# Kernel optimization log

Hardware: AMD Instinct MI355X
Metric: run time of the kernel (lower is better)

The kernel has to match this reference:

```python
import jax, jax.numpy as jnp
import numpy as np

B, D, NB, E, DT, K, TS = 16384, 512, 8, 4, 256, 8, 16
GH = max(D // 2, 16)            # gate hidden = 256
SH = max(int(DT * 0.5), 16)     # safe head hidden = 128
SPD = DT + TS                   # spec head input = 272
SPH = max(int(SPD * 0.25), 16)  # spec hidden = 68
CFD = DT + 1 + 3 + TS + 1 + 1   # conf input = 278
CFH = max(int(CFD * 0.25), 16)  # conf hidden = 69


def _ln(x, g, b):
    m = x.mean(-1, keepdims=True)
    v = ((x - m) ** 2).mean(-1, keepdims=True)
    return (x - m) / jnp.sqrt(v + 1e-5) * g + b


def _resmlp(x, lg, lb, W1, b1, W2, b2):
    h = jax.nn.relu(_ln(x, lg, lb) @ W1 + b1)
    return h @ W2 + b2


def setup_inputs() -> dict:
    key = jax.random.key(0)
    ks = iter(jax.random.split(key, 48))

    def n(shape, s=0.02):
        return (jax.random.normal(next(ks), shape, jnp.float32) * s).astype(jnp.float32)

    inp = {
        'x_num': jax.random.normal(next(ks), (B, D), jnp.float32),
        # GGPLNumericEmbedding
        'basis_weight': n((D, NB + 1, E), 0.001),
        'basis_bias': jnp.zeros((D, E), jnp.float32),
        'bp_min': jnp.zeros((D, 1), jnp.float32),
        'bp_delta_raw': n((D, NB), 0.1),
        'proj_W': n((D * E, D)), 'proj_b': jnp.zeros((D,), jnp.float32),
        # input gate MLP
        'gate_W1': n((D, GH)), 'gate_b1': jnp.zeros((GH,), jnp.float32),
        'gate_W2': n((GH, D)), 'gate_b2': jnp.zeros((D,), jnp.float32),
        # backbone stand-in (TMLPBackbone.encode_hidden): 2-layer MLP -> d_token
        'bb_W1': n((D, DT)), 'bb_b1': jnp.zeros((DT,), jnp.float32),
        'bb_W2': n((DT, DT)), 'bb_b2': jnp.zeros((DT,), jnp.float32),
        # base head
        'base_W': n((DT, 1)), 'base_b': jnp.zeros((1,), jnp.float32),
        # safe residual head (zero_last=True -> zero last weight)
        'safe_ln_g': jnp.ones((DT,), jnp.float32), 'safe_ln_b': jnp.zeros((DT,), jnp.float32),
        'safe_W1': n((DT, SH)), 'safe_b1': jnp.zeros((SH,), jnp.float32),
        'safe_W2': jnp.zeros((SH, 1), jnp.float32), 'safe_b2': jnp.zeros((1,), jnp.float32),
        # top feature summary
        'top_W1': n((1, TS), 0.001), 'top_b1': jnp.zeros((TS,), jnp.float32),
        'top_W2': n((TS, TS), 0.001), 'top_b2': jnp.zeros((TS,), jnp.float32),
        # spec head
        'spec_ln_g': jnp.ones((SPD,), jnp.float32), 'spec_ln_b': jnp.zeros((SPD,), jnp.float32),
        'spec_W1': n((SPD, SPH)), 'spec_b1': jnp.zeros((SPH,), jnp.float32),
        'spec_W2': n((SPH, 1), 0.001), 'spec_b2': jnp.zeros((1,), jnp.float32),
        # conf gate (last bias init = -2.0)
        'conf_ln_g': jnp.ones((CFD,), jnp.float32), 'conf_ln_b': jnp.zeros((CFD,), jnp.float32),
        'conf_W1': n((CFD, CFH)), 'conf_b1': jnp.zeros((CFH,), jnp.float32),
        'conf_W2': n((CFH, 1), 0.001), 'conf_b2': jnp.full((1,), -2.0, jnp.float32),
    }
    return inp


def reference(x_num, basis_weight, basis_bias, bp_min, bp_delta_raw, proj_W, proj_b,
              gate_W1, gate_b1, gate_W2, gate_b2, bb_W1, bb_b1, bb_W2, bb_b2,
              base_W, base_b, safe_ln_g, safe_ln_b, safe_W1, safe_b1, safe_W2, safe_b2,
              top_W1, top_b1, top_W2, top_b2, spec_ln_g, spec_ln_b, spec_W1, spec_b1,
              spec_W2, spec_b2, conf_ln_g, conf_ln_b, conf_W1, conf_b1, conf_W2, conf_b2):
    # --- GGPL numeric embedding ---
    bps = bp_min + jnp.cumsum(jax.nn.softplus(bp_delta_raw), axis=1)        # [D, NB]
    basis = jnp.concatenate([x_num[..., None],
                             jax.nn.relu(x_num[..., None] - bps[None])], -1)  # [B, D, NB+1]
    emb = jnp.einsum('bdf,dfe->bde', basis, basis_weight) + basis_bias       # [B, D, E]
    flat = emb.reshape(x_num.shape[0], -1)
    x_in = x_num + 0.1 * (flat @ proj_W + proj_b)
    # --- input gate ---
    g = jax.nn.sigmoid(jax.nn.relu(x_in @ gate_W1 + gate_b1) @ gate_W2 + gate_b2)
    x_gated = x_in * g
    # --- backbone + base head ---
    h = jax.nn.relu(jax.nn.relu(x_gated @ bb_W1 + bb_b1) @ bb_W2 + bb_b2)    # [B, DT]
    y_base = h @ base_W + base_b                                             # [B, 1]
    # --- gate stats (population std, matching unbiased=False) ---
    gmean = g.mean(1, keepdims=True)
    gmax = g.max(1, keepdims=True)
    gstd = g.std(1, keepdims=True)
    # --- safe residual head ---
    delta_safe = _resmlp(h, safe_ln_g, safe_ln_b, safe_W1, safe_b1, safe_W2, safe_b2)
    # --- top-k gate selection + gather ---
    topk_g, topk_idx = jax.lax.top_k(g, K)                                   # [B, K]
    topk_x = jnp.take_along_axis(x_in, topk_idx, axis=1)
    topk_w = topk_g / (topk_g.sum(1, keepdims=True) + 1e-6)
    xw = (topk_x * topk_w)[..., None]                                        # [B, K, 1]
    tokens = jax.nn.relu(xw @ top_W1 + top_b1) @ top_W2 + top_b2             # [B, K, TS]
    z_top = tokens.mean(1)                                                   # [B, TS]
    # --- spec head + confidence gate ---
    delta_spec = _resmlp(jnp.concatenate([h, z_top], 1),
                         spec_ln_g, spec_ln_b, spec_W1, spec_b1, spec_W2, spec_b2)
    conf_in = jnp.concatenate([h, y_base, gmean, gmax, gstd, z_top,
                               jnp.abs(delta_safe), jnp.abs(delta_spec)], 1)
    gamma = jax.nn.sigmoid(_resmlp(conf_in, conf_ln_g, conf_ln_b,
                                   conf_W1, conf_b1, conf_W2, conf_b2))
    y_hat = y_base + delta_safe + gamma * delta_spec
    return y_hat.squeeze(-1)                                                 # [B]
```

## Files before the change

kernel.cpp:

```cpp
#include <hip/hip_runtime.h>
#include <cstddef>

typedef unsigned short u16;
typedef unsigned int   u32;
typedef short bf16x8 __attribute__((ext_vector_type(8)));
typedef float f32x4 __attribute__((ext_vector_type(4)));

#define B_ROWS 16384
#define D_FEAT 512
#define NB_    8

static __device__ __forceinline__ float b2f(u16 h) {
    union { u32 u; float f; } v; v.u = ((u32)h) << 16; return v.f;
}
static __device__ __forceinline__ u16 f2b(float f) {
    union { float f; u32 u; } v; v.f = f;
    u32 r = (v.u + 0x7fffu + ((v.u >> 16) & 1u)) >> 16;
    return (u16)r;
}
static __device__ __forceinline__ float ldf(const void* p, size_t i, int isb) {
    return isb ? b2f(((const u16*)p)[i]) : ((const float*)p)[i];
}
static __device__ __forceinline__ u16 cvtb(const void* p, size_t i, int isb) {
    return isb ? ((const u16*)p)[i] : f2b(((const float*)p)[i]);
}
static __device__ __forceinline__ float wred_sum(float v) {
    #pragma unroll
    for (int off = 32; off > 0; off >>= 1) v += __shfl_xor(v, off);
    return v;
}
static __device__ __forceinline__ float wred_max(float v) {
    #pragma unroll
    for (int off = 32; off > 0; off >>= 1) v = fmaxf(v, __shfl_xor(v, off));
    return v;
}
static __device__ __forceinline__ void async_copy16(const u16* g, u16* l) {
    __builtin_amdgcn_global_load_lds(
        (const __attribute__((address_space(1))) u32*)g,
        (__attribute__((address_space(3))) u32*)l, 16, 0, 0);
}

#define WO_PROJ 0
#define WO_GW1  1048576
#define WO_GW2  1179648
#define WO_BW1  1310720
#define WO_BW2  1441792
#define WO_SW1  1507328
#define WO_SPW  1540096
#define WO_CFW  1581056
#define W_TOTAL 1622016
#define NB_REPACK 6336

struct PrepArgs {
    const void *xnum;
    const void *pW, *gW1, *gW2, *bW1, *bW2, *sW1, *spW, *cfW;
    const void *pb, *g1, *g2, *b1, *b2, *sb, *spb, *cfb;
    const void *bwt, *bbias, *bp_min, *bp_dr;
    u16 *Wbuf; float *biasbuf, *bwT, *bbT, *bpsT;
    int *flag;
};

__global__ __launch_bounds__(256) void prep_all_k(PrepArgs P) {
    __shared__ int s_isb;
    if (threadIdx.x < 64) {
        int lane = threadIdx.x;
        u16 h = ((const u16*)P.xnum)[lane * 2];
        int e = (h >> 7) & 0xff;
        unsigned long long m = __ballot(e >= 110 && e <= 132);
        if (lane == 0) s_isb = (__popcll(m) >= 32) ? 1 : 0;
    }
    __syncthreads();
    const int isb = s_isb;
    const int bid = blockIdx.x;
    const int tid = threadIdx.x;

    if (bid < NB_REPACK) {
        size_t t = (size_t)bid * 256 + tid;
        u16 v;
        if (t < WO_GW1) {
            size_t i = t; int n = (int)(i >> 11), k = (int)(i & 2047);
            v = cvtb(P.pW, (size_t)k * 512 + n, isb);
        } else if (t < WO_GW2) {
            size_t i = t - WO_GW1; int n = (int)(i >> 9), k = (int)(i & 511);
            v = cvtb(P.gW1, (size_t)k * 256 + n, isb);
        } else if (t < WO_BW1) {
            size_t i = t - WO_GW2; int n = (int)(i >> 8), k = (int)(i & 255);
            v = cvtb(P.gW2, (size_t)k * 512 + n, isb);
        } else if (t < WO_BW2) {
            size_t i = t - WO_BW1; int n = (int)(i >> 9), k = (int)(i & 511);
            v = cvtb(P.bW1, (size_t)k * 256 + n, isb);
        } else if (t < WO_SW1) {
            size_t i = t - WO_BW2; int n = (int)(i >> 8), k = (int)(i & 255);
            v = cvtb(P.bW2, (size_t)k * 256 + n, isb);
        } else if (t < WO_SPW) {
            size_t i = t - WO_SW1; int n = (int)(i >> 8), k = (int)(i & 255);
            v = cvtb(P.sW1, (size_t)k * 128 + n, isb);
        } else if (t < WO_CFW) {
            size_t i = t - WO_SPW; int n = (int)(i / 320), k = (int)(i % 320);
            v = (n < 68 && k < 272) ? cvtb(P.spW, (size_t)k * 68 + n, isb) : (u16)0;
        } else {
            size_t i = t - WO_CFW; int n = (int)(i / 320), k = (int)(i % 320);
            v = (n < 69 && k < 278) ? cvtb(P.cfW, (size_t)k * 69 + n, isb) : (u16)0;
        }
        P.Wbuf[t] = v;
    } else if (bid < NB_REPACK + 9) {
        int t = (bid - NB_REPACK) * 256 + tid;
        float* out = P.biasbuf;
        if      (t < 512)  out[t] = ldf(P.pb, t, isb);
        else if (t < 768)  out[t] = ldf(P.g1, t - 512, isb);
        else if (t < 1280) out[t] = ldf(P.g2, t - 768, isb);
        else if (t < 1536) out[t] = ldf(P.b1, t - 1280, isb);
        else if (t < 1792) out[t] = ldf(P.b2, t - 1536, isb);
        else if (t < 1920) out[t] = ldf(P.sb, t - 1792, isb);
        else if (t < 2048) { int c = t - 1920; out[t] = (c < 68) ? ldf(P.spb, c, isb) : 0.f; }
        else if (t < 2176) { int c = t - 2048; out[t] = (c < 69) ? ldf(P.cfb, c, isb) : 0.f; }
    } else if (bid < NB_REPACK + 9 + 72) {
        int t = (bid - NB_REPACK - 9) * 256 + tid;
        if (t < 512 * 36) {
            int d = t / 36, j = t % 36;
            P.bwT[j * 512 + d] = ldf(P.bwt, t, isb);
        }
        if (t < 2048) {
            int d = t >> 2, e = t & 3;
            P.bbT[e * 512 + d] = ldf(P.bbias, t, isb);
        }
    } else {
        int d = (bid - NB_REPACK - 9 - 72) * 256 + tid;
        if (d < D_FEAT) {
            float bp = ldf(P.bp_min, d, isb);
            #pragma unroll
            for (int k = 0; k < NB_; ++k) {
                float x = ldf(P.bp_dr, d * NB_ + k, isb);
                bp += fmaxf(x, 0.f) + log1pf(expf(-fabsf(x)));
                P.bpsT[k * 512 + d] = bp;
            }
        }
        if (d == 0) *P.flag = isb;
    }
}

__global__ __launch_bounds__(256) void emb_k(
    const void* __restrict__ xnum, const float* __restrict__ bwT,
    const float* __restrict__ bbT, const float* __restrict__ bpsT,
    u16* __restrict__ emb, const int* __restrict__ flag, int rowoff)
{
    const int isb = *flag;
    size_t gi = ((size_t)blockIdx.x * 256 + threadIdx.x) * 4;
    int d0 = (int)(gi & 511);
    float xv[4];
    if (isb) {
        u16 tmp[4];
        *(uint2*)tmp = *(const uint2*)((const u16*)xnum + (size_t)rowoff * 512 + gi);
        #pragma unroll
        for (int i = 0; i < 4; ++i) xv[i] = b2f(tmp[i]);
    } else {
        float4 f = *(const float4*)((const float*)xnum + (size_t)rowoff * 512 + gi);
        xv[0] = f.x; xv[1] = f.y; xv[2] = f.z; xv[3] = f.w;
    }
    float acc[4][4];
    #pragma unroll
    for (int e = 0; e < 4; ++e) {
        float4 b = *(const float4*)&bbT[e * 512 + d0];
        acc[0][e] = b.x; acc[1][e] = b.y; acc[2][e] = b.z; acc[3][e] = b.w;
    }
    #pragma unroll
    for (int f = 0; f <= 8; ++f) {
        float bv[4];
        if (f == 0) {
            #pragma unroll
            for (int i = 0; i < 4; ++i) bv[i] = xv[i];
        } else {
            float4 bp = *(const float4*)&bpsT[(f - 1) * 512 + d0];
            bv[0] = fmaxf(xv[0] - bp.x, 0.f); bv[1] = fmaxf(xv[1] - bp.y, 0.f);
            bv[2] = fmaxf(xv[2] - bp.z, 0.f); bv[3] = fmaxf(xv[3] - bp.w, 0.f);
        }
        #pragma unroll
        for (int e = 0; e < 4; ++e) {
            float4 w = *(const float4*)&bwT[(f * 4 + e) * 512 + d0];
            acc[0][e] = fmaf(bv[0], w.x, acc[0][e]);
            acc[1][e] = fmaf(bv[1], w.y, acc[1][e]);
            acc[2][e] = fmaf(bv[2], w.z, acc[2][e]);
            acc[3][e] = fmaf(bv[3], w.w, acc[3][e]);
        }
    }
    u16 o[16];
    #pragma unroll
    for (int i = 0; i < 4; ++i)
        #pragma unroll
        for (int e = 0; e < 4; ++e) o[i * 4 + e] = f2b(acc[i][e]);
    *(uint4*)&emb[gi * 4]     = *(const uint4*)&o[0];
    *(uint4*)&emb[gi * 4 + 8] = *(const uint4*)&o[8];
}

template<int EMODE>
__global__ __launch_bounds__(256) void mgemm_k(
    const u16* __restrict__ A, const u16* __restrict__ Bt,
    const float* __restrict__ bias,
    void* __restrict__ out0, const void* __restrict__ aux0, void* __restrict__ aux1,
    int N, int Kdim, int lda, int ldk, int rowoff, const int* __restrict__ flagp)
{
    __shared__ __align__(16) u16 As[2][64][64];
    __shared__ __align__(16) u16 Bs[2][64][64];

    const int isb = (EMODE == 0) ? *flagp : 0;
    const int tid = threadIdx.x;
    const int row0 = blockIdx.x * 64, col0 = blockIdx.y * 64;
    const int w = tid >> 6, lane = tid & 63, q = lane >> 4, mr = lane & 15;
    const int wr = (w >> 1) * 32, wc = (w & 1) * 32;
    const int rr = lane >> 3, kg = lane & 7;
    const int sc = kg ^ (rr & 7);

    f32x4 acc[2][2];
    #pragma unroll
    for (int a = 0; a < 2; ++a)
        #pragma unroll
        for (int b = 0; b < 2; ++b) acc[a][b] = (f32x4){0.f, 0.f, 0.f, 0.f};

    const int T = Kdim >> 6;

    auto stage = [&](int kt, int bi) {
        if (w < 2) {
            #pragma unroll
            for (int j = 0; j < 4; ++j) {
                int m = w * 32 + j * 8;
                async_copy16(A + (size_t)(row0 + m + rr) * lda + kt + sc * 8,
                             &As[bi][m][0]);
            }
        } else {
            #pragma unroll
            for (int j = 0; j < 4; ++j) {
                int m = (w - 2) * 32 + j * 8;
                async_copy16(Bt + (size_t)(col0 + m + rr) * ldk + kt + sc * 8,
                             &Bs[bi][m][0]);
            }
        }
    };

    stage(0, 0);
    __syncthreads();

    for (int t = 0; t < T; ++t) {
        if (t + 1 < T) stage((t + 1) << 6, (t + 1) & 1);
        const int cb = t & 1;
        #pragma unroll
        for (int ks = 0; ks < 2; ++ks) {
            bf16x8 af[2], bf[2];
            #pragma unroll
            for (int rs = 0; rs < 2; ++rs) {
                int r = wr + rs * 16 + mr;
                int pc = (ks * 4 + q) ^ (r & 7);
                af[rs] = *(const bf16x8*)&As[cb][r][pc * 8];
            }
            #pragma unroll
            for (int nt = 0; nt < 2; ++nt) {
                int r = wc + nt * 16 + mr;
                int pc = (ks * 4 + q) ^ (r & 7);
                bf[nt] = *(const bf16x8*)&Bs[cb][r][pc * 8];
            }
            #pragma unroll
            for (int rs = 0; rs < 2; ++rs)
                #pragma unroll
                for (int nt = 0; nt < 2; ++nt)
                    acc[rs][nt] = __builtin_amdgcn_mfma_f32_16x16x32_bf16(
                        af[rs], bf[nt], acc[rs][nt], 0, 0, 0);
        }
        __syncthreads();
    }

    #pragma unroll
    for (int rs = 0; rs < 2; ++rs) {
        #pragma unroll
        for (int i = 0; i < 4; ++i) {
            size_t gr = (size_t)rowoff + row0 + wr + rs * 16 + q * 4 + i;
            #pragma unroll
            for (int nt = 0; nt < 2; ++nt) {
                int c = col0 + wc + nt * 16 + mr;
                float z = acc[rs][nt][i] + bias[c];
                size_t idx = gr * (size_t)N + c;
                if (EMODE == 0) {
                    ((u16*)out0)[idx] = f2b(ldf(aux0, idx, isb) + 0.1f * z);
                } else if (EMODE == 1) {
                    ((u16*)out0)[idx] = f2b(fmaxf(z, 0.f));
                } else {
                    float gv = 1.f / (1.f + expf(-z));
                    ((u16*)out0)[idx] = f2b(gv);
                    ((u16*)aux1)[idx] = f2b(b2f(((const u16*)aux0)[idx]) * gv);
                }
            }
        }
    }
}

struct PreArgs {
    const u16 *x_in, *g, *h;
    const void *base_W, *base_b;
    const void *safe_ln_g, *safe_ln_b;
    const void *top_W1, *top_b1, *top_W2, *top_b2;
    const void *spec_ln_g, *spec_ln_b;
    u16 *ln_a, *ln_b;
    float *scal;
    const int *flag;
};

__global__ __launch_bounds__(256, 4) void pre_k(PreArgs P) {
    __shared__ float w_base[256], w_slg[256], w_slb[256], w_t2[256];
    __shared__ float w_plg[272], w_plb[272];
    __shared__ float w_t1[16], w_tb1[16], w_tb2[16];
    const int isb = *P.flag;
    const int tid = threadIdx.x;
    const int wid = tid >> 6;
    const int lane = tid & 63;
    const int row = blockIdx.x * 4 + wid;

    w_base[tid] = ldf(P.base_W, tid, isb);
    w_slg[tid]  = ldf(P.safe_ln_g, tid, isb);
    w_slb[tid]  = ldf(P.safe_ln_b, tid, isb);
    w_t2[tid]   = ldf(P.top_W2, tid, isb);
    if (tid < 272) {
        w_plg[tid] = ldf(P.spec_ln_g, tid, isb);
        w_plb[tid] = ldf(P.spec_ln_b, tid, isb);
    }
    if (tid < 16) {
        w_t1[tid]  = ldf(P.top_W1, tid, isb);
        w_tb1[tid] = ldf(P.top_b1, tid, isb);
        w_tb2[tid] = ldf(P.top_b2, tid, isb);
    }
    __syncthreads();

    float hv[4], gv[8];
    #pragma unroll
    for (int i = 0; i < 4; ++i) hv[i] = b2f(P.h[(size_t)row * 256 + lane + 64 * i]);
    #pragma unroll
    for (int j = 0; j < 8; ++j) gv[j] = b2f(P.g[(size_t)row * 512 + lane + 64 * j]);
    const float hsum = hv[0] + hv[1] + hv[2] + hv[3];

    float pb = 0.f;
    #pragma unroll
    for (int i = 0; i < 4; ++i) pb = fmaf(hv[i], w_base[lane + 64 * i], pb);
    const float yb = wred_sum(pb) + ldf(P.base_b, 0, isb);

    float s1 = 0.f, s2 = 0.f, mx = -1e30f;
    #pragma unroll
    for (int j = 0; j < 8; ++j) { s1 += gv[j]; s2 = fmaf(gv[j], gv[j], s2); mx = fmaxf(mx, gv[j]); }
    s1 = wred_sum(s1); s2 = wred_sum(s2); mx = wred_max(mx);
    const float gmean = s1 * (1.f / 512.f);
    const float gstd = sqrtf(fmaxf(s2 * (1.f / 512.f) - gmean * gmean, 0.f));

    const float hm = wred_sum(hsum) * (1.f / 256.f);
    float pv = 0.f;
    #pragma unroll
    for (int i = 0; i < 4; ++i) { float d = hv[i] - hm; pv = fmaf(d, d, pv); }
    const float hrstd = rsqrtf(wred_sum(pv) * (1.f / 256.f) + 1e-5f);
    #pragma unroll
    for (int i = 0; i < 4; ++i) {
        int k = lane + 64 * i;
        P.ln_a[(size_t)row * 320 + k] = f2b((hv[i] - hm) * hrstd * w_slg[k] + w_slb[k]);
    }

    float tg[8];
    #pragma unroll
    for (int j = 0; j < 8; ++j) tg[j] = gv[j];
    float myv = 0.f, sumtv = 0.f; int myi = 0;
    for (int r8 = 0; r8 < 8; ++r8) {
        float bv = -1e30f; int bi = 0x7fffffff;
        #pragma unroll
        for (int j = 0; j < 8; ++j) {
            int idx = lane + 64 * j;
            if (tg[j] > bv || (tg[j] == bv && idx < bi)) { bv = tg[j]; bi = idx; }
        }
        #pragma unroll
        for (int off = 32; off > 0; off >>= 1) {
            float ov = __shfl_xor(bv, off);
            int oi = __shfl_xor(bi, off);
            if (ov > bv || (ov == bv && oi < bi)) { bv = ov; bi = oi; }
        }
        sumtv += bv;
        if (lane == r8) { myv = bv; myi = bi; }
        if ((bi & 63) == lane) {
            int oj = bi >> 6;
            #pragma unroll
            for (int j = 0; j < 8; ++j) if (j == oj) tg[j] = -1e30f;
        }
    }

    float th[16];
    #pragma unroll
    for (int s = 0; s < 16; ++s) th[s] = 0.f;
    if (lane < 8) {
        float xi = b2f(P.x_in[(size_t)row * 512 + myi]);
        float xw = xi * (myv / (sumtv + 1e-6f));
        #pragma unroll
        for (int s = 0; s < 16; ++s)
            th[s] = fmaxf(fmaf(xw, w_t1[s], w_tb1[s]), 0.f);
    }
    #pragma unroll
    for (int s = 0; s < 16; ++s) {
        th[s] += __shfl_xor(th[s], 1);
        th[s] += __shfl_xor(th[s], 2);
        th[s] += __shfl_xor(th[s], 4);
    }
    const int tt = lane & 15;
    float zacc = w_tb2[tt];
    #pragma unroll
    for (int s = 0; s < 16; ++s)
        zacc = fmaf(__shfl(th[s], 0), w_t2[s * 16 + tt], zacc);
    const float ztl = zacc * 0.125f;

    float ps = hsum + ((lane < 16) ? ztl : 0.f);
    const float sm = wred_sum(ps) * (1.f / 272.f);
    float pv2 = 0.f;
    #pragma unroll
    for (int i = 0; i < 4; ++i) { float d = hv[i] - sm; pv2 = fmaf(d, d, pv2); }
    if (lane < 16) { float d = ztl - sm; pv2 = fmaf(d, d, pv2); }
    const float srstd = rsqrtf(wred_sum(pv2) * (1.f / 272.f) + 1e-5f);
    #pragma unroll
    for (int i = 0; i < 4; ++i) {
        int k = lane + 64 * i;
        P.ln_b[(size_t)row * 320 + k] = f2b((hv[i] - sm) * srstd * w_plg[k] + w_plb[k]);
    }
    if (lane < 16) {
        int k = 256 + lane;
        P.ln_b[(size_t)row * 320 + k] = f2b((ztl - sm) * srstd * w_plg[k] + w_plb[k]);
    } else {
        P.ln_b[(size_t)row * 320 + 256 + lane] = 0;
    }

    float* sc = P.scal + (size_t)row * 32;
    if (lane < 16) sc[8 + lane] = ztl;
    if (lane == 0) { sc[0] = yb; sc[1] = gmean; sc[2] = mx; sc[3] = gstd; }
}

struct MidArgs {
    const u16 *h;
    const float *scal_in;
    const u16 *sh, *sph;
    const void *safe_W2, *safe_b2, *spec_W2, *spec_b2;
    const void *conf_ln_g, *conf_ln_b;
    u16 *ln_c;
    float *scal;
    const int *flag;
};

__global__ __launch_bounds__(256, 4) void mid_k(MidArgs P) {
    __shared__ float w_clg[278], w_clb[278], w_sw2[128], w_spw2[68];
    const int isb = *P.flag;
    const int tid = threadIdx.x;
    const int wid = tid >> 6;
    const int lane = tid & 63;
    const int row = blockIdx.x * 4 + wid;

    if (tid < 278) { w_clg[tid] = ldf(P.conf_ln_g, tid, isb); w_clb[tid] = ldf(P.conf_ln_b, tid, isb); }
    if (tid < 128) w_sw2[tid]  = ldf(P.safe_W2, tid, isb);
    if (tid < 68)  w_spw2[tid] = ldf(P.spec_W2, tid, isb);
    __syncthreads();

    float s0 = b2f(P.sh[(size_t)row * 128 + lane]);
    float s1 = b2f(P.sh[(size_t)row * 128 + 64 + lane]);
    float psafe = s0 * w_sw2[lane] + s1 * w_sw2[64 + lane];
    const float dsafe = wred_sum(psafe) + ldf(P.safe_b2, 0, isb);

    float p0 = b2f(P.sph[(size_t)row * 128 + lane]) * ((lane < 68) ? w_spw2[lane] : 0.f);
    if (lane < 4) p0 += b2f(P.sph[(size_t)row * 128 + 64 + lane]) * w_spw2[64 + lane];
    const float dspec = wred_sum(p0) + ldf(P.spec_b2, 0, isb);

    const float* sc = P.scal_in + (size_t)row * 32;
    const float yb = sc[0], gmean = sc[1], mx = sc[2], gstd = sc[3];
    const float ztl = (lane < 16) ? sc[8 + lane] : 0.f;

    float hv[4];
    #pragma unroll
    for (int i = 0; i < 4; ++i) hv[i] = b2f(P.h[(size_t)row * 256 + lane + 64 * i]);
    const float hsum = hv[0] + hv[1] + hv[2] + hv[3];

    const float ads = fabsf(dsafe), adsp = fabsf(dspec);
    float pc = hsum + ((lane < 16) ? ztl : 0.f)
             + ((lane == 0) ? (yb + gmean + mx + gstd + ads + adsp) : 0.f);
    const float cm = wred_sum(pc) * (1.f / 278.f);
    float pv3 = 0.f;
    #pragma unroll
    for (int i = 0; i < 4; ++i) { float d = hv[i] - cm; pv3 = fmaf(d, d, pv3); }
    if (lane < 16) { float d = ztl - cm; pv3 = fmaf(d, d, pv3); }
    if (lane == 0) {
        float vals[6] = { yb, gmean, mx, gstd, ads, adsp };
        #pragma unroll
        for (int q = 0; q < 6; ++q) { float d = vals[q] - cm; pv3 = fmaf(d, d, pv3); }
    }
    const float crstd = rsqrtf(wred_sum(pv3) * (1.f / 278.f) + 1e-5f);

    u16* la = P.ln_c + (size_t)row * 320;
    #pragma unroll
    for (int i = 0; i < 4; ++i) {
        int k = lane + 64 * i;
        la[k] = f2b((hv[i] - cm) * crstd * w_clg[k] + w_clb[k]);
    }
    if (lane < 16) {
        int k = 260 + lane;
        la[k] = f2b((ztl - cm) * crstd * w_clg[k] + w_clb[k]);
    } else if (lane >= 18 && lane < 60) {
        la[260 + lane] = 0;
    }
    if (lane == 0) {
        float vals[6] = { yb, gmean, mx, gstd, ads, adsp };
        int idxs[6] = { 256, 257, 258, 259, 276, 277 };
        #pragma unroll
        for (int q = 0; q < 6; ++q) {
            int k = idxs[q];
            la[k] = f2b((vals[q] - cm) * crstd * w_clg[k] + w_clb[k]);
        }
        float* so = P.scal + (size_t)row * 32;
        so[4] = dsafe; so[5] = dspec;
    }
}

__global__ __launch_bounds__(256, 4) void post_k(
    const u16* __restrict__ ch, const float* __restrict__ scal,
    const void* __restrict__ conf_W2, const void* __restrict__ conf_b2,
    void* __restrict__ out, const int* __restrict__ flag)
{
    __shared__ float w_cw2[69];
    const int isb = *flag;
    const int tid = threadIdx.x;
    const int wid = tid >> 6;
    const int lane = tid & 63;
    const int row = blockIdx.x * 4 + wid;

    if (tid < 69) w_cw2[tid] = ldf(conf_W2, tid, isb);
    __syncthreads();

    float c0 = b2f(ch[(size_t)row * 128 + lane]) * ((lane < 69) ? w_cw2[lane] : 0.f);
    if (lane < 5) c0 += b2f(ch[(size_t)row * 128 + 64 + lane]) * w_cw2[64 + lane];
    const float zlin = wred_sum(c0) + ldf(conf_b2, 0, isb);
    const float gamma = 1.f / (1.f + expf(-zlin));
    if (lane == 0) {
        const float* sc = scal + (size_t)row * 32;
        float v = sc[0] + sc[4] + gamma * sc[5];
        if (isb) ((u16*)out)[row] = f2b(v);
        else     ((float*)out)[row] = v;
    }
}

extern "C" void kernel_launch(void* const* d_in, const int* in_sizes, int n_in,
                              void* d_out, int out_size, void* d_ws, size_t ws_size,
                              hipStream_t stream) {
    (void)in_sizes; (void)n_in; (void)out_size; (void)ws_size;
    const void* x_num = d_in[0];

    char* p = (char*)d_ws;
    auto alloc = [&](size_t bytes) { char* r = p; p += (bytes + 15) & ~(size_t)15; return r; };

    int*   flag    = (int*)alloc(16);
    float* bpsT    = (float*)alloc(8 * 512 * 4);
    float* bwT     = (float*)alloc(36 * 512 * 4);
    float* bbT     = (float*)alloc(4 * 512 * 4);
    float* biasbuf = (float*)alloc(2176 * 4);
    u16*   Wbuf    = (u16*)alloc((size_t)W_TOTAL * 2);
    u16*   ebuf    = (u16*)alloc((size_t)(B_ROWS / 2) * 2048 * 2);
    u16*   x_in    = (u16*)alloc((size_t)B_ROWS * 512 * 2);
    u16*   hid1    = (u16*)alloc((size_t)B_ROWS * 256 * 2);
    u16*   hbuf    = (u16*)alloc((size_t)B_ROWS * 256 * 2);
    u16*   ln_a    = (u16*)alloc((size_t)B_ROWS * 320 * 2);
    u16*   ln_b    = (u16*)alloc((size_t)B_ROWS * 320 * 2);
    float* scal    = (float*)alloc((size_t)B_ROWS * 32 * 4);
    u16*   sh      = (u16*)alloc((size_t)B_ROWS * 128 * 2);
    u16*   sph     = (u16*)alloc((size_t)B_ROWS * 128 * 2);
    u16*   xg      = (u16*)alloc((size_t)B_ROWS * 512 * 2);
    u16*   hid2    = (u16*)alloc((size_t)B_ROWS * 256 * 2);

    u16*   g   = ebuf;
    u16*   chh = hid1;

    {
        PrepArgs pr;
        pr.xnum = x_num;
        pr.pW = d_in[5];  pr.gW1 = d_in[7];  pr.gW2 = d_in[9];
        pr.bW1 = d_in[11]; pr.bW2 = d_in[13]; pr.sW1 = d_in[19];
        pr.spW = d_in[29]; pr.cfW = d_in[35];
        pr.pb = d_in[6];  pr.g1 = d_in[8];  pr.g2 = d_in[10];
        pr.b1 = d_in[12]; pr.b2 = d_in[14]; pr.sb = d_in[20];
        pr.spb = d_in[30]; pr.cfb = d_in[36];
        pr.bwt = d_in[1]; pr.bbias = d_in[2];
        pr.bp_min = d_in[3]; pr.bp_dr = d_in[4];
        pr.Wbuf = Wbuf; pr.biasbuf = biasbuf;
        pr.bwT = bwT; pr.bbT = bbT; pr.bpsT = bpsT;
        pr.flag = flag;
        prep_all_k<<<NB_REPACK + 9 + 72 + 2, 256, 0, stream>>>(pr);
    }

    const int HR = B_ROWS / 2;
    for (int half = 0; half < 2; ++half) {
        int rowoff = half * HR;
        emb_k<<<(HR * D_FEAT / 4) / 256, 256, 0, stream>>>(
            x_num, bwT, bbT, bpsT, ebuf, flag, rowoff);
        mgemm_k<0><<<dim3(HR / 64, 8), 256, 0, stream>>>(
            ebuf, Wbuf + WO_PROJ, biasbuf + 0, x_in, x_num, nullptr,
            512, 2048, 2048, 2048, rowoff, flag);
    }

    mgemm_k<1><<<dim3(B_ROWS / 64, 4), 256, 0, stream>>>(
        x_in, Wbuf + WO_GW1, biasbuf + 512, hid1, nullptr, nullptr,
        256, 512, 512, 512, 0, flag);
    mgemm_k<2><<<dim3(B_ROWS / 64, 8), 256, 0, stream>>>(
        hid1, Wbuf + WO_GW2, biasbuf + 768, g, x_in, xg,
        512, 256, 256, 256, 0, flag);
    mgemm_k<1><<<dim3(B_ROWS / 64, 4), 256, 0, stream>>>(
        xg, Wbuf + WO_BW1, biasbuf + 1280, hid2, nullptr, nullptr,
        256, 512, 512, 512, 0, flag);
    mgemm_k<1><<<dim3(B_ROWS / 64, 4), 256, 0, stream>>>(
        hid2, Wbuf + WO_BW2, biasbuf + 1536, hbuf, nullptr, nullptr,
        256, 256, 256, 256, 0, flag);

    {
        PreArgs pa;
        pa.x_in = x_in; pa.g = g; pa.h = hbuf;
        pa.base_W = d_in[15]; pa.base_b = d_in[16];
        pa.safe_ln_g = d_in[17]; pa.safe_ln_b = d_in[18];
        pa.top_W1 = d_in[23]; pa.top_b1 = d_in[24];
        pa.top_W2 = d_in[25]; pa.top_b2 = d_in[26];
        pa.spec_ln_g = d_in[27]; pa.spec_ln_b = d_in[28];
        pa.ln_a = ln_a; pa.ln_b = ln_b; pa.scal = scal; pa.flag = flag;
        pre_k<<<B_ROWS / 4, 256, 0, stream>>>(pa);
    }

    mgemm_k<1><<<dim3(B_ROWS / 64, 2), 256, 0, stream>>>(
        ln_a, Wbuf + WO_SW1, biasbuf + 1792, sh, nullptr, nullptr,
        128, 256, 320, 256, 0, flag);
    mgemm_k<1><<<dim3(B_ROWS / 64, 2), 256, 0, stream>>>(
        ln_b, Wbuf + WO_SPW, biasbuf + 1920, sph, nullptr, nullptr,
        128, 320, 320, 320, 0, flag);

    {
        MidArgs ma;
        ma.h = hbuf; ma.scal_in = scal; ma.sh = sh; ma.sph = sph;
        ma.safe_W2 = d_in[21]; ma.safe_b2 = d_in[22];
        ma.spec_W2 = d_in[31]; ma.spec_b2 = d_in[32];
        ma.conf_ln_g = d_in[33]; ma.conf_ln_b = d_in[34];
        ma.ln_c = ln_a; ma.scal = scal; ma.flag = flag;
        mid_k<<<B_ROWS / 4, 256, 0, stream>>>(ma);
    }

    mgemm_k<1><<<dim3(B_ROWS / 64, 2), 256, 0, stream>>>(
        ln_a, Wbuf + WO_CFW, biasbuf + 2048, chh, nullptr, nullptr,
        128, 320, 320, 320, 0, flag);

    post_k<<<B_ROWS / 4, 256, 0, stream>>>(chh, scal, d_in[37], d_in[38], d_out, flag);
}
```

Measured before the change: 454.0 us.

## Tile-transpose weight repack via LDS and batch safe/spec GEMMs in one launch

The per-element strided weight transpose in the prep kernel is replaced with a dedicated 64x64 LDS-tiled transpose kernel, so that both the reads and the writes of the large weight matrices are coalesced. The two independent small GEMMs for the safe and spec heads are merged into a single launch with a doubled grid, which removes one kernel launch and its tail. The tradeoffs are an extra kernel launch for the transpose and a duplicated GEMM kernel body.

```diff
diff --git a/kernel.cpp b/kernel.cpp
--- a/kernel.cpp
+++ b/kernel.cpp
@@ -38,6 +38,13 @@
     __builtin_amdgcn_global_load_lds(
         (const __attribute__((address_space(1))) u32*)g,
         (__attribute__((address_space(3))) u32*)l, 16, 0, 0);
+}
+static __device__ __forceinline__ int detect_isb(const void* xnum) {
+    int lane = threadIdx.x & 63;
+    u16 h = ((const u16*)xnum)[lane * 2];
+    int e = (h >> 7) & 0xff;
+    unsigned long long m = __ballot(e >= 110 && e <= 132);
+    return (__popcll(m) >= 32) ? 1 : 0;
 }
 
 #define WO_PROJ 0
@@ -49,11 +56,57 @@
 #define WO_SPW  1540096
 #define WO_CFW  1581056
 #define W_TOTAL 1622016
-#define NB_REPACK 6336
-
+
+struct TransArgs {
+    const void *xnum;
+    const void *src[6];
+    u16 *Wbuf;
+};
+
+__global__ __launch_bounds__(256) void transW_k(TransArgs P) {
+    __shared__ int s_isb;
+    __shared__ u16 tile[64][68];
+    if (threadIdx.x < 64) { int r = detect_isb(P.xnum); if ((threadIdx.x & 63) == 0) s_isb = r; }
+    __syncthreads();
+    const int isb = s_isb;
+    const int tid = threadIdx.x;
+
+    const int Ks[6]   = {2048, 512, 256, 512, 256, 256};
+    const int Nss[6]  = {512, 256, 512, 256, 256, 128};
+    const int offs[6] = {WO_PROJ, WO_GW1, WO_GW2, WO_BW1, WO_BW2, WO_SW1};
+
+    int bid = blockIdx.x, m = 0;
+    #pragma unroll
+    for (int i = 0; i < 6; ++i) {
+        int nt = (Ks[i] >> 6) * (Nss[i] >> 6);
+        if (bid >= nt && m == i) { bid -= nt; m = i + 1; }
+    }
+    const int K = Ks[m], N = Nss[m];
+    const int ktiles = K >> 6;
+    const int tn = bid / ktiles, tk = bid % ktiles;
+    const int k0 = tk * 64, n0 = tn * 64;
+    const void* src = P.src[m];
+    u16* dst = P.Wbuf + offs[m];
+
+    #pragma unroll
+    for (int p = 0; p < 16; ++p) {
+        int kk = p * 4 + (tid >> 6);
+        int nn = tid & 63;
+        tile[kk][nn] = cvtb(src, (size_t)(k0 + kk) * N + n0 + nn, isb);
+    }
+    __syncthreads();
+    #pragma unroll
+    for (int p = 0; p < 16; ++p) {
+        int nn = p * 4 + (tid >> 6);
+        int kk = tid & 63;
+        dst[(size_t)(n0 + nn) * K + k0 + kk] = tile[kk][nn];
+    }
+}
+
+#define NB_SPW 160
 struct PrepArgs {
     const void *xnum;
-    const void *pW, *gW1, *gW2, *bW1, *bW2, *sW1, *spW, *cfW;
+    const void *spW, *cfW;
     const void *pb, *g1, *g2, *b1, *b2, *sb, *spb, *cfb;
     const void *bwt, *bbias, *bp_min, *bp_dr;
     u16 *Wbuf; float *biasbuf, *bwT, *bbT, *bpsT;
@@ -62,49 +115,24 @@
 
 __global__ __launch_bounds__(256) void prep_all_k(PrepArgs P) {
     __shared__ int s_isb;
-    if (threadIdx.x < 64) {
-        int lane = threadIdx.x;
-        u16 h = ((const u16*)P.xnum)[lane * 2];
-        int e = (h >> 7) & 0xff;
-        unsigned long long m = __ballot(e >= 110 && e <= 132);
-        if (lane == 0) s_isb = (__popcll(m) >= 32) ? 1 : 0;
-    }
+    if (threadIdx.x < 64) { int r = detect_isb(P.xnum); if ((threadIdx.x & 63) == 0) s_isb = r; }
     __syncthreads();
     const int isb = s_isb;
     const int bid = blockIdx.x;
     const int tid = threadIdx.x;
 
-    if (bid < NB_REPACK) {
-        size_t t = (size_t)bid * 256 + tid;
-        u16 v;
-        if (t < WO_GW1) {
-            size_t i = t; int n = (int)(i >> 11), k = (int)(i & 2047);
-            v = cvtb(P.pW, (size_t)k * 512 + n, isb);
-        } else if (t < WO_GW2) {
-            size_t i = t - WO_GW1; int n = (int)(i >> 9), k = (int)(i & 511);
-            v = cvtb(P.gW1, (size_t)k * 256 + n, isb);
-        } else if (t < WO_BW1) {
-            size_t i = t - WO_GW2; int n = (int)(i >> 8), k = (int)(i & 255);
-            v = cvtb(P.gW2, (size_t)k * 512 + n, isb);
-        } else if (t < WO_BW2) {
-            size_t i = t - WO_BW1; int n = (int)(i >> 9), k = (int)(i & 511);
-            v = cvtb(P.bW1, (size_t)k * 256 + n, isb);
-        } else if (t < WO_SW1) {
-            size_t i = t - WO_BW2; int n = (int)(i >> 8), k = (int)(i & 255);
-            v = cvtb(P.bW2, (size_t)k * 256 + n, isb);
-        } else if (t < WO_SPW) {
-            size_t i = t - WO_SW1; int n = (int)(i >> 8), k = (int)(i & 255);
-            v = cvtb(P.sW1, (size_t)k * 128 + n, isb);
-        } else if (t < WO_CFW) {
-            size_t i = t - WO_SPW; int n = (int)(i / 320), k = (int)(i % 320);
-            v = (n < 68 && k < 272) ? cvtb(P.spW, (size_t)k * 68 + n, isb) : (u16)0;
-        } else {
-            size_t i = t - WO_CFW; int n = (int)(i / 320), k = (int)(i % 320);
-            v = (n < 69 && k < 278) ? cvtb(P.cfW, (size_t)k * 69 + n, isb) : (u16)0;
-        }
-        P.Wbuf[t] = v;
-    } else if (bid < NB_REPACK + 9) {
-        int t = (bid - NB_REPACK) * 256 + tid;
+    if (bid < NB_SPW) {
+        size_t i = (size_t)bid * 256 + tid;
+        int n = (int)(i / 320), k = (int)(i % 320);
+        P.Wbuf[WO_SPW + i] =
+            (n < 68 && k < 272) ? cvtb(P.spW, (size_t)k * 68 + n, isb) : (u16)0;
+    } else if (bid < 2 * NB_SPW) {
+        size_t i = (size_t)(bid - NB_SPW) * 256 + tid;
+        int n = (int)(i / 320), k = (int)(i % 320);
+        P.Wbuf[WO_CFW + i] =
+            (n < 69 && k < 278) ? cvtb(P.cfW, (size_t)k * 69 + n, isb) : (u16)0;
+    } else if (bid < 2 * NB_SPW + 9) {
+        int t = (bid - 2 * NB_SPW) * 256 + tid;
         float* out = P.biasbuf;
         if      (t < 512)  out[t] = ldf(P.pb, t, isb);
         else if (t < 768)  out[t] = ldf(P.g1, t - 512, isb);
@@ -114,8 +142,8 @@
         else if (t < 1920) out[t] = ldf(P.sb, t - 1792, isb);
         else if (t < 2048) { int c = t - 1920; out[t] = (c < 68) ? ldf(P.spb, c, isb) : 0.f; }
         else if (t < 2176) { int c = t - 2048; out[t] = (c < 69) ? ldf(P.cfb, c, isb) : 0.f; }
-    } else if (bid < NB_REPACK + 9 + 72) {
-        int t = (bid - NB_REPACK - 9) * 256 + tid;
+    } else if (bid < 2 * NB_SPW + 9 + 72) {
+        int t = (bid - 2 * NB_SPW - 9) * 256 + tid;
         if (t < 512 * 36) {
             int d = t / 36, j = t % 36;
             P.bwT[j * 512 + d] = ldf(P.bwt, t, isb);
@@ -125,7 +153,7 @@
             P.bbT[e * 512 + d] = ldf(P.bbias, t, isb);
         }
     } else {
-        int d = (bid - NB_REPACK - 9 - 72) * 256 + tid;
+        int d = (bid - 2 * NB_SPW - 9 - 72) * 256 + tid;
         if (d < D_FEAT) {
             float bp = ldf(P.bp_min, d, isb);
             #pragma unroll
@@ -286,6 +314,106 @@
                     ((u16*)out0)[idx] = f2b(gv);
                     ((u16*)aux1)[idx] = f2b(b2f(((const u16*)aux0)[idx]) * gv);
                 }
+            }
+        }
+    }
+}
+
+__global__ __launch_bounds__(256) void mgemm_pair_k(
+    const u16* __restrict__ A1, const u16* __restrict__ B1,
+    const float* __restrict__ bias1, u16* __restrict__ out1,
+    int K1, int lda1, int ldk1,
+    const u16* __restrict__ A2, const u16* __restrict__ B2,
+    const float* __restrict__ bias2, u16* __restrict__ out2,
+    int K2, int lda2, int ldk2,
+    int N, int nx1)
+{
+    __shared__ __align__(16) u16 As[2][64][64];
+    __shared__ __align__(16) u16 Bs[2][64][64];
+
+    const int tid = threadIdx.x;
+    const bool sec = blockIdx.x >= nx1;
+    const u16* A = sec ? A2 : A1;
+    const u16* Bt = sec ? B2 : B1;
+    const float* bias = sec ? bias2 : bias1;
+    u16* out0 = sec ? out2 : out1;
+    const int Kdim = sec ? K2 : K1;
+    const int lda = sec ? lda2 : lda1;
+    const int ldk = sec ? ldk2 : ldk1;
+    const int row0 = (sec ? blockIdx.x - nx1 : blockIdx.x) * 64;
+    const int col0 = blockIdx.y * 64;
+    const int w = tid >> 6, lane = tid & 63, q = lane >> 4, mr = lane & 15;
+    const int wr = (w >> 1) * 32, wc = (w & 1) * 32;
+    const int rr = lane >> 3, kg = lane & 7;
+    const int sc = kg ^ (rr & 7);
+
+    f32x4 acc[2][2];
+    #pragma unroll
+    for (int a = 0; a < 2; ++a)
+        #pragma unroll
+        for (int b = 0; b < 2; ++b) acc[a][b] = (f32x4){0.f, 0.f, 0.f, 0.f};
+
+    const int T = Kdim >> 6;
+
+    auto stage = [&](int kt, int bi) {
+        if (w < 2) {
+            #pragma unroll
+            for (int j = 0; j < 4; ++j) {
+                int m = w * 32 + j * 8;
+                async_copy16(A + (size_t)(row0 + m + rr) * lda + kt + sc * 8,
+                             &As[bi][m][0]);
+            }
+        } else {
+            #pragma unroll
+            for (int j = 0; j < 4; ++j) {
+                int m = (w - 2) * 32 + j * 8;
+                async_copy16(Bt + (size_t)(col0 + m + rr) * ldk + kt + sc * 8,
+                             &Bs[bi][m][0]);
+            }
+        }
+    };
+
+    stage(0, 0);
+    __syncthreads();
+
+    for (int t = 0; t < T; ++t) {
+        if (t + 1 < T) stage((t + 1) << 6, (t + 1) & 1);
+        const int cb = t & 1;
+        #pragma unroll
+        for (int ks = 0; ks < 2; ++ks) {
+            bf16x8 af[2], bf[2];
+            #pragma unroll
+            for (int rs = 0; rs < 2; ++rs) {
+                int r = wr + rs * 16 + mr;
+                int pc = (ks * 4 + q) ^ (r & 7);
+                af[rs] = *(const bf16x8*)&As[cb][r][pc * 8];
+            }
+            #pragma unroll
+            for (int nt = 0; nt < 2; ++nt) {
+                int r = wc + nt * 16 + mr;
+                int pc = (ks * 4 + q) ^ (r & 7);
+                bf[nt] = *(const bf16x8*)&Bs[cb][r][pc * 8];
+            }
+            #pragma unroll
+            for (int rs = 0; rs < 2; ++rs)
+                #pragma unroll
+                for (int nt = 0; nt < 2; ++nt)
+                    acc[rs][nt] = __builtin_amdgcn_mfma_f32_16x16x32_bf16(
+                        af[rs], bf[nt], acc[rs][nt], 0, 0, 0);
+        }
+        __syncthreads();
+    }
+
+    #pragma unroll
+    for (int rs = 0; rs < 2; ++rs) {
+        #pragma unroll
+        for (int i = 0; i < 4; ++i) {
+            size_t gr = (size_t)row0 + wr + rs * 16 + q * 4 + i;
+            #pragma unroll
+            for (int nt = 0; nt < 2; ++nt) {
+                int c = col0 + wc + nt * 16 + mr;
+                float z = acc[rs][nt][i] + bias[c];
+                out0[gr * (size_t)N + c] = f2b(fmaxf(z, 0.f));
             }
         }
     }
@@ -572,8 +700,6 @@
     {
         PrepArgs pr;
         pr.xnum = x_num;
-        pr.pW = d_in[5];  pr.gW1 = d_in[7];  pr.gW2 = d_in[9];
-        pr.bW1 = d_in[11]; pr.bW2 = d_in[13]; pr.sW1 = d_in[19];
         pr.spW = d_in[29]; pr.cfW = d_in[35];
         pr.pb = d_in[6];  pr.g1 = d_in[8];  pr.g2 = d_in[10];
         pr.b1 = d_in[12]; pr.b2 = d_in[14]; pr.sb = d_in[20];
@@ -583,7 +709,14 @@
         pr.Wbuf = Wbuf; pr.biasbuf = biasbuf;
         pr.bwT = bwT; pr.bbT = bbT; pr.bpsT = bpsT;
         pr.flag = flag;
-        prep_all_k<<<NB_REPACK + 9 + 72 + 2, 256, 0, stream>>>(pr);
+        prep_all_k<<<2 * NB_SPW + 9 + 72 + 2, 256, 0, stream>>>(pr);
+
+        TransArgs tr;
+        tr.xnum = x_num;
+        tr.src[0] = d_in[5];  tr.src[1] = d_in[7];  tr.src[2] = d_in[9];
+        tr.src[3] = d_in[11]; tr.src[4] = d_in[13]; tr.src[5] = d_in[19];
+        tr.Wbuf = Wbuf;
+        transW_k<<<376, 256, 0, stream>>>(tr);
     }
 
     const int HR = B_ROWS / 2;
@@ -621,12 +754,10 @@
         pre_k<<<B_ROWS / 4, 256, 0, stream>>>(pa);
     }
 
-    mgemm_k<1><<<dim3(B_ROWS / 64, 2), 256, 0, stream>>>(
-        ln_a, Wbuf + WO_SW1, biasbuf + 1792, sh, nullptr, nullptr,
-        128, 256, 320, 256, 0, flag);
-    mgemm_k<1><<<dim3(B_ROWS / 64, 2), 256, 0, stream>>>(
-        ln_b, Wbuf + WO_SPW, biasbuf + 1920, sph, nullptr, nullptr,
-        128, 320, 320, 320, 0, flag);
+    mgemm_pair_k<<<dim3(2 * (B_ROWS / 64), 2), 256, 0, stream>>>(
+        ln_a, Wbuf + WO_SW1, biasbuf + 1792, sh, 256, 320, 256,
+        ln_b, Wbuf + WO_SPW, biasbuf + 1920, sph, 320, 320, 320,
+        128, B_ROWS / 64);
 
     {
         MidArgs ma;
```

Result: no change. 451.2 us (-0.6%).
